# Kernel optimization log

Hardware: AMD Instinct MI355X
Metric: run time of the kernel (lower is better)

Reference implementation:

```python
import jax, jax.numpy as jnp
import numpy as np

B, T, C = 2, 2048, 1024
H = 16
D = C // H  # 64
SCALE = 1.0 / np.sqrt(D)


def setup_inputs() -> dict:
    key = jax.random.key(0)
    k1, k2, k3 = jax.random.split(key, 3)
    x = jax.random.normal(k1, (B, T, C), dtype=jnp.float32)
    Wqkv = jax.random.normal(k2, (C, 3 * C), dtype=jnp.float32) * 0.02
    bqkv = jnp.zeros((3 * C,), dtype=jnp.float32)
    Wo = jax.random.normal(k3, (C, C), dtype=jnp.float32) * 0.02
    bo = jnp.zeros((C,), dtype=jnp.float32)
    return {"x": x, "Wqkv": Wqkv, "bqkv": bqkv, "Wo": Wo, "bo": bo}


def reference(x, Wqkv, bqkv, Wo, bo):
    Bsz, Tlen, Cdim = x.shape
    qkv = x @ Wqkv + bqkv                       # [B,T,3C]
    qkv = qkv.reshape(Bsz, Tlen, 3, H, D)
    qkv = jnp.transpose(qkv, (2, 0, 3, 1, 4))   # [3,B,H,T,D]
    q, k, v = qkv[0], qkv[1], qkv[2]
    att = jnp.einsum("bhqd,bhkd->bhqk", q, k) * SCALE
    # NOTE: faithful to source: mask keeps positions where k >= q
    i = jnp.arange(Tlen)
    mask = i[None, :] >= i[:, None]             # [T,T], entry [q,k]: k >= q
    att = jnp.where(mask[None, None], att, -jnp.inf)
    att = jax.nn.softmax(att, axis=-1)
    # dropout p=0.0 (inference) -> identity
    y = jnp.einsum("bhqk,bhkd->bhqd", att, v)   # [B,H,T,D]
    y = jnp.transpose(y, (0, 2, 1, 3)).reshape(Bsz, Tlen, Cdim)
    y = y @ Wo + bo
    return y
```

## Files before the change

kernel.cpp:

```cpp
#include <hip/hip_runtime.h>
#include <hip/hip_bf16.h>
#include <cstdint>
#include <cstddef>

typedef __bf16 bf16_t;
typedef __bf16 bf16x8 __attribute__((ext_vector_type(8)));
typedef __bf16 bf16x4 __attribute__((ext_vector_type(4)));
typedef short short4v __attribute__((ext_vector_type(4)));
typedef float f32x4 __attribute__((ext_vector_type(4)));

#define NB 2
#define NT 2048
#define NC 1024
#define NH 16
#define ND 64
#define NM (NB * NT)
#define N3 (3 * NC)
#define QSCALE_LOG2E 0.18033688011112042f

#define GLOAD_LDS16(gptr, lptr)                                                          \
  __builtin_amdgcn_global_load_lds((const __attribute__((address_space(1))) void*)(gptr), \
                                   (__attribute__((address_space(3))) void*)(lptr), 16, 0, 0)

__global__ __launch_bounds__(256) void prep_k(const float* __restrict__ x,
                                              const float* __restrict__ Wqkv,
                                              const float* __restrict__ Wo,
                                              bf16_t* __restrict__ xbf,
                                              bf16_t* __restrict__ wqkvT,
                                              bf16_t* __restrict__ woT) {
  __shared__ float tile[32][33];
  const int bx = blockIdx.x;
  if (bx < 4096) {
    const int i = (bx * 256 + threadIdx.x) * 4;
    const float4 v = *(const float4*)(x + i);
    bf16x4 o;
    o[0] = (bf16_t)v.x; o[1] = (bf16_t)v.y; o[2] = (bf16_t)v.z; o[3] = (bf16_t)v.w;
    *(bf16x4*)(xbf + i) = o;
    return;
  }
  const int t = bx - 4096;
  const int cxi = t & 127;
  const int tr = (t >> 7) * 32;
  const float* in;
  bf16_t* out;
  int Ccols, tc;
  if (cxi < 96) { in = Wqkv; out = wqkvT; Ccols = 3072; tc = cxi * 32; }
  else          { in = Wo;   out = woT;   Ccols = 1024; tc = (cxi - 96) * 32; }
  const int lx = threadIdx.x & 31;
  const int ly = threadIdx.x >> 5;
#pragma unroll
  for (int i = 0; i < 32; i += 8)
    tile[ly + i][lx] = in[(size_t)(tr + ly + i) * Ccols + tc + lx];
  __syncthreads();
#pragma unroll
  for (int i = 0; i < 32; i += 8)
    out[(size_t)(tc + ly + i) * 1024 + tr + lx] = (bf16_t)tile[lx][ly + i];
}

__global__ __launch_bounds__(256) void qkv_gemm_k(const bf16_t* __restrict__ A,
                                                  const bf16_t* __restrict__ Bt,
                                                  const float* __restrict__ bias,
                                                  bf16_t* __restrict__ qb,
                                                  bf16_t* __restrict__ kb,
                                                  bf16_t* __restrict__ vt2) {
  __shared__ __align__(16) bf16_t lds[16384];
  bf16_t* As = lds;
  bf16_t* Bs = lds + 8192;
  const int xcd = blockIdx.x & 7;
  const int i2 = blockIdx.x >> 3;
  const int m0 = (i2 & 31) * 128;
  const int n0 = (xcd * 3 + (i2 >> 5)) * 128;

  const int lane = threadIdx.x & 63;
  const int w = threadIdx.x >> 6;
  const int wm = (w & 1) * 64, wn = (w >> 1) * 64;
  const int quad = lane >> 4, l16 = lane & 15;
  const int sw = l16 & 7;

  f32x4 acc[4][4] = {};

  for (int k0 = 0; k0 < NC; k0 += 64) {
#pragma unroll
    for (int i = 0; i < 4; ++i) {
      const int gb = w * 256 + i * 64;
      const int g = gb + lane;
      const int row = g >> 3;
      const int cs = (g & 7) ^ (row & 7);
      GLOAD_LDS16(A + (size_t)(m0 + row) * NC + k0 + cs * 8, As + gb * 8);
      GLOAD_LDS16(Bt + (size_t)(n0 + row) * NC + k0 + cs * 8, Bs + gb * 8);
    }
    __syncthreads();
#pragma unroll
    for (int h = 0; h < 2; ++h) {
      bf16x8 af[4], bfr[4];
#pragma unroll
      for (int i = 0; i < 4; ++i)
        af[i] = *(const bf16x8*)(As + ((wm + i * 16 + l16) * 8 + ((h * 4 + quad) ^ sw)) * 8);
#pragma unroll
      for (int j = 0; j < 4; ++j)
        bfr[j] = *(const bf16x8*)(Bs + ((wn + j * 16 + l16) * 8 + ((h * 4 + quad) ^ sw)) * 8);
#pragma unroll
      for (int i = 0; i < 4; ++i)
#pragma unroll
        for (int j = 0; j < 4; ++j)
          acc[i][j] = __builtin_amdgcn_mfma_f32_16x16x32_bf16(af[i], bfr[j], acc[i][j], 0, 0, 0);
    }
    __syncthreads();
  }

#pragma unroll
  for (int i = 0; i < 4; ++i)
#pragma unroll
    for (int j = 0; j < 4; ++j) {
      const int n = n0 + wn + j * 16 + l16;
      const float bn = bias[n];
      const int which = n >> 10;
      const int rem = n & 1023;
      const int h = rem >> 6, d = rem & 63;
      const int mb = m0 + wm + i * 16 + quad * 4;
      const int b = mb >> 11, t4 = mb & 2047;
      const size_t bh = (size_t)b * NH + h;
      if (which == 2) {
        const int c = t4 >> 6, g = (t4 >> 2) & 15;
        bf16x4 val;
#pragma unroll
        for (int r = 0; r < 4; ++r) val[r] = (bf16_t)(acc[i][j][r] + bn);
        *(bf16x4*)(vt2 + ((bh * 32 + c) * 1024 + (size_t)g * 64 + d) * 4) = val;
      } else {
        bf16_t* dst = (which == 0) ? qb : kb;
        const float sc = (which == 0) ? QSCALE_LOG2E : 1.0f;
#pragma unroll
        for (int r = 0; r < 4; ++r)
          dst[(bh * NT + t4 + r) * ND + d] = (bf16_t)((acc[i][j][r] + bn) * sc);
      }
    }
}

__global__ __launch_bounds__(256, 4) void attn_k(const bf16_t* __restrict__ q,
                                                 const bf16_t* __restrict__ k,
                                                 const bf16_t* __restrict__ vt2,
                                                 bf16_t* __restrict__ y ) {
  const int bh = blockIdx.x & 31;
  const int u = (blockIdx.x >> 5) & 7;
  const int r4 = blockIdx.x >> 8;
  const int T = r4 * 8 + ((r4 & 1) ? (7 - u) : u);
  const int b = bh >> 4, h = bh & 15;

  const bf16_t* qp = q + (size_t)bh * NT * ND;
  const bf16_t* kp = k + (size_t)bh * NT * ND;
  const bf16_t* vp = vt2 + (size_t)bh * 32 * 4096;

  __shared__ __align__(16) bf16_t kbuf0[4096], kbuf1[4096];
  __shared__ __align__(16) bf16_t vbuf0[4096], vbuf1[4096];

  const int lane = threadIdx.x & 63;
  const int w = threadIdx.x >> 6;
  const int quad = lane >> 4, l16 = lane & 15;
  const int qv = T * 64 + w * 16 + l16;

  const bf16x8 qf0 = *(const bf16x8*)(qp + (size_t)qv * ND + quad * 8);
  const bf16x8 qf1 = *(const bf16x8*)(qp + (size_t)qv * ND + 32 + quad * 8);

  const short4v ones = {0x3F80, 0x3F80, 0x3F80, 0x3F80};

  f32x4 zs = {0.f, 0.f, 0.f, 0.f};
  f32x4 o[4];
#pragma unroll
  for (int dj = 0; dj < 4; ++dj) o[dj] = (f32x4){0.f, 0.f, 0.f, 0.f};

  auto stage = [&](int c, bf16_t* kb_, bf16_t* vb_) {
    const bf16_t* kc = kp + (size_t)c * 4096;
    const bf16_t* vc = vp + (size_t)c * 4096;
#pragma unroll
    for (int i = 0; i < 2; ++i) {
      const int gb = w * 128 + i * 64;
      const int s = gb + lane;
      const int row = s >> 3;
      const int cs = (s & 7) ^ (row & 7);
      GLOAD_LDS16(kc + (size_t)row * 64 + cs * 8, kb_ + gb * 8);
      GLOAD_LDS16(vc + (size_t)s * 8, vb_ + gb * 8);
    }
  };

  auto step = [&](const bf16_t* kt, const bf16_t* vt, int c) {
    const int t0 = c * 64;
    f32x4 sv[4];
#pragma unroll
    for (int kj = 0; kj < 4; ++kj) {
      const int kr = kj * 16 + l16;
      const int sw = kr & 7;
      const bf16x8 a0 = *(const bf16x8*)(kt + ((size_t)kr * 8 + (quad ^ sw)) * 8);
      const bf16x8 a1 = *(const bf16x8*)(kt + ((size_t)kr * 8 + ((4 + quad) ^ sw)) * 8);
      f32x4 z = {0.f, 0.f, 0.f, 0.f};
      z = __builtin_amdgcn_mfma_f32_16x16x32_bf16(a0, qf0, z, 0, 0, 0);
      z = __builtin_amdgcn_mfma_f32_16x16x32_bf16(a1, qf1, z, 0, 0, 0);
      sv[kj] = z;
    }
    if (c == T) {
#pragma unroll
      for (int kj = 0; kj < 4; ++kj)
#pragma unroll
        for (int r = 0; r < 4; ++r)
          if (t0 + kj * 16 + quad * 4 + r < qv) sv[kj][r] = -INFINITY;
    }
    short4v pf[4];
#pragma unroll
    for (int kj = 0; kj < 4; ++kj) {
      bf16x4 pb;
#pragma unroll
      for (int r = 0; r < 4; ++r) pb[r] = (bf16_t)__builtin_amdgcn_exp2f(sv[kj][r]);
      pf[kj] = __builtin_bit_cast(short4v, pb);
    }
#pragma unroll
    for (int kj = 0; kj < 4; ++kj)
      zs = __builtin_amdgcn_mfma_f32_16x16x16bf16_1k(ones, pf[kj], zs, 0, 0, 0);
#pragma unroll
    for (int dj = 0; dj < 4; ++dj) {
#pragma unroll
      for (int kj = 0; kj < 4; ++kj) {
        const bf16x4 a =
            *(const bf16x4*)(vt + ((size_t)(kj * 4 + quad) * 64 + dj * 16 + l16) * 4);
        o[dj] = __builtin_amdgcn_mfma_f32_16x16x16bf16_1k(
            __builtin_bit_cast(short4v, a), pf[kj], o[dj], 0, 0, 0);
      }
    }
  };

  stage(T, kbuf0, vbuf0);
  int c = T;
  while (true) {
    __syncthreads();
    if (c + 1 < 32) stage(c + 1, kbuf1, vbuf1);
    step(kbuf0, vbuf0, c);
    if (++c >= 32) break;
    __syncthreads();
    if (c + 1 < 32) stage(c + 1, kbuf0, vbuf0);
    step(kbuf1, vbuf1, c);
    if (++c >= 32) break;
  }

  const float inv = 1.0f / zs[0];
  const size_t base = ((size_t)b * NT + qv) * NC + h * 64;
#pragma unroll
  for (int dj = 0; dj < 4; ++dj) {
    bf16x4 va;
#pragma unroll
    for (int r = 0; r < 4; ++r) va[r] = (bf16_t)(o[dj][r] * inv);
    *(bf16x4*)(y + base + dj * 16 + quad * 4) = va;
  }
}

__global__ __launch_bounds__(256) void out_gemm_k(const bf16_t* __restrict__ A,
                                                  const bf16_t* __restrict__ Bt,
                                                  const float* __restrict__ bias,
                                                  float* __restrict__ out) {
  __shared__ __align__(16) bf16_t lds[6144];
  bf16_t* As = lds;
  bf16_t* Bs = lds + 2048;
  const int n0 = (blockIdx.x & 7) * 128;
  const int m0 = (blockIdx.x >> 3) * 64;

  const int lane = threadIdx.x & 63;
  const int w = threadIdx.x >> 6;
  const int wm = (w & 1) * 32, wn = (w >> 1) * 64;
  const int quad = lane >> 4, l16 = lane & 15;

  f32x4 acc[2][4] = {};

  for (int k0 = 0; k0 < NC; k0 += 32) {
    {
      const int g = w * 64 + lane;
      GLOAD_LDS16(A + (size_t)(m0 + (g >> 2)) * NC + k0 + (g & 3) * 8, As + w * 64 * 8);
    }
#pragma unroll
    for (int i = 0; i < 2; ++i) {
      const int gb = w * 128 + i * 64;
      const int g = gb + lane;
      GLOAD_LDS16(Bt + (size_t)(n0 + (g >> 2)) * NC + k0 + (g & 3) * 8, Bs + gb * 8);
    }
    __syncthreads();
    bf16x8 af[2], bfr[4];
#pragma unroll
    for (int i = 0; i < 2; ++i)
      af[i] = *(const bf16x8*)(As + ((wm + i * 16 + l16) * 4 + quad) * 8);
#pragma unroll
    for (int j = 0; j < 4; ++j)
      bfr[j] = *(const bf16x8*)(Bs + ((wn + j * 16 + l16) * 4 + quad) * 8);
#pragma unroll
    for (int i = 0; i < 2; ++i)
#pragma unroll
      for (int j = 0; j < 4; ++j)
        acc[i][j] = __builtin_amdgcn_mfma_f32_16x16x32_bf16(af[i], bfr[j], acc[i][j], 0, 0, 0);
    __syncthreads();
  }

#pragma unroll
  for (int i = 0; i < 2; ++i)
#pragma unroll
    for (int j = 0; j < 4; ++j) {
      const int n = n0 + wn + j * 16 + l16;
      const float bn = bias[n];
#pragma unroll
      for (int r = 0; r < 4; ++r) {
        const int m = m0 + wm + i * 16 + quad * 4 + r;
        out[(size_t)m * NC + n] = acc[i][j][r] + bn;
      }
    }
}

extern "C" void kernel_launch(void* const* d_in, const int* in_sizes, int n_in,
                              void* d_out, int out_size, void* d_ws, size_t ws_size,
                              hipStream_t stream) {
  const float* x = (const float*)d_in[0];
  const float* Wqkv = (const float*)d_in[1];
  const float* bqkv = (const float*)d_in[2];
  const float* Wo = (const float*)d_in[3];
  const float* bo = (const float*)d_in[4];
  float* out = (float*)d_out;

  char* p = (char*)d_ws;
  bf16_t* xbf = (bf16_t*)p;   p += (size_t)NM * NC * sizeof(bf16_t);
  bf16_t* wqkvT = (bf16_t*)p; p += (size_t)N3 * NC * sizeof(bf16_t);
  bf16_t* woT = (bf16_t*)p;   p += (size_t)NC * NC * sizeof(bf16_t);
  bf16_t* qb = (bf16_t*)p;    p += (size_t)NB * NH * NT * ND * sizeof(bf16_t);
  bf16_t* kb = (bf16_t*)p;    p += (size_t)NB * NH * NT * ND * sizeof(bf16_t);
  bf16_t* vt2 = (bf16_t*)p;   p += (size_t)NB * NH * NT * ND * sizeof(bf16_t);
  bf16_t* yb = (bf16_t*)p;    p += (size_t)NM * NC * sizeof(bf16_t);

  hipLaunchKernelGGL(prep_k, dim3(8192), dim3(256), 0, stream,
                     x, Wqkv, Wo, xbf, wqkvT, woT);
  hipLaunchKernelGGL(qkv_gemm_k, dim3(768), dim3(256), 0, stream,
                     xbf, wqkvT, bqkv, qb, kb, vt2);
  hipLaunchKernelGGL(attn_k, dim3(1024), dim3(256), 0, stream, qb, kb, vt2, yb);
  hipLaunchKernelGGL(out_gemm_k, dim3(512), dim3(256), 0, stream,
                     yb, woT, bo, out);
}
```

Before: 177.8 us.

## Double-buffer QKV GEMM LDS tiles with K-step of 32

Restructures the QKV projection GEMM main loop to ping-pong between two LDS buffers, issuing the global-to-LDS loads for the next K-slice before computing on the current one. The K-step shrinks from 64 to 32, and the XOR swizzle on LDS rows is dropped in favour of a plain 32-element row layout. The goal is to hide global load latency behind MFMA work and cut one barrier per iteration. The trade-off is twice as many loop iterations with less MFMA work each, and possible LDS bank conflicts now that the swizzle is gone.

```diff
diff --git a/kernel.cpp b/kernel.cpp
--- a/kernel.cpp
+++ b/kernel.cpp
@@ -63,9 +63,7 @@
                                                   bf16_t* __restrict__ qb,
                                                   bf16_t* __restrict__ kb,
                                                   bf16_t* __restrict__ vt2) {
-  __shared__ __align__(16) bf16_t lds[16384];
-  bf16_t* As = lds;
-  bf16_t* Bs = lds + 8192;
+  __shared__ __align__(16) bf16_t As0[4096], Bs0[4096], As1[4096], Bs1[4096];
   const int xcd = blockIdx.x & 7;
   const int i2 = blockIdx.x >> 3;
   const int m0 = (i2 & 31) * 128;
@@ -75,37 +73,45 @@
   const int w = threadIdx.x >> 6;
   const int wm = (w & 1) * 64, wn = (w >> 1) * 64;
   const int quad = lane >> 4, l16 = lane & 15;
-  const int sw = l16 & 7;
 
   f32x4 acc[4][4] = {};
 
-  for (int k0 = 0; k0 < NC; k0 += 64) {
-#pragma unroll
-    for (int i = 0; i < 4; ++i) {
-      const int gb = w * 256 + i * 64;
+  auto stage = [&](int k0, bf16_t* As_, bf16_t* Bs_) {
+#pragma unroll
+    for (int i = 0; i < 2; ++i) {
+      const int gb = w * 128 + i * 64;
       const int g = gb + lane;
-      const int row = g >> 3;
-      const int cs = (g & 7) ^ (row & 7);
-      GLOAD_LDS16(A + (size_t)(m0 + row) * NC + k0 + cs * 8, As + gb * 8);
-      GLOAD_LDS16(Bt + (size_t)(n0 + row) * NC + k0 + cs * 8, Bs + gb * 8);
-    }
-    __syncthreads();
-#pragma unroll
-    for (int h = 0; h < 2; ++h) {
-      bf16x8 af[4], bfr[4];
-#pragma unroll
-      for (int i = 0; i < 4; ++i)
-        af[i] = *(const bf16x8*)(As + ((wm + i * 16 + l16) * 8 + ((h * 4 + quad) ^ sw)) * 8);
+      GLOAD_LDS16(A + (size_t)(m0 + (g >> 2)) * NC + k0 + (g & 3) * 8, As_ + gb * 8);
+      GLOAD_LDS16(Bt + (size_t)(n0 + (g >> 2)) * NC + k0 + (g & 3) * 8, Bs_ + gb * 8);
+    }
+  };
+
+  auto compute = [&](const bf16_t* As_, const bf16_t* Bs_) {
+    bf16x8 af[4], bfr[4];
+#pragma unroll
+    for (int i = 0; i < 4; ++i)
+      af[i] = *(const bf16x8*)(As_ + (wm + i * 16 + l16) * 32 + quad * 8);
+#pragma unroll
+    for (int j = 0; j < 4; ++j)
+      bfr[j] = *(const bf16x8*)(Bs_ + (wn + j * 16 + l16) * 32 + quad * 8);
+#pragma unroll
+    for (int i = 0; i < 4; ++i)
 #pragma unroll
       for (int j = 0; j < 4; ++j)
-        bfr[j] = *(const bf16x8*)(Bs + ((wn + j * 16 + l16) * 8 + ((h * 4 + quad) ^ sw)) * 8);
-#pragma unroll
-      for (int i = 0; i < 4; ++i)
-#pragma unroll
-        for (int j = 0; j < 4; ++j)
-          acc[i][j] = __builtin_amdgcn_mfma_f32_16x16x32_bf16(af[i], bfr[j], acc[i][j], 0, 0, 0);
-    }
-    __syncthreads();
+        acc[i][j] = __builtin_amdgcn_mfma_f32_16x16x32_bf16(af[i], bfr[j], acc[i][j], 0, 0, 0);
+  };
+
+  stage(0, As0, Bs0);
+  int k0 = 0;
+  while (true) {
+    __syncthreads();
+    if (k0 + 32 < NC) stage(k0 + 32, As1, Bs1);
+    compute(As0, Bs0);
+    k0 += 32; if (k0 >= NC) break;
+    __syncthreads();
+    if (k0 + 32 < NC) stage(k0 + 32, As0, Bs0);
+    compute(As1, Bs1);
+    k0 += 32; if (k0 >= NC) break;
   }
 
 #pragma unroll
```

New measurement: 164.1 us. -7.7%, faster.
